# Optimization experiments

Measured on AMD Instinct MI355X. Metric: run time of the kernel, lower is better.

Reference implementation:

```python
import jax, jax.numpy as jnp
import numpy as np

K_TOP = 4          # self.k
NUM_EXPERTS = 16   # self.num_experts
LOSS_COEF = 0.01


def setup_inputs() -> dict:
    key = jax.random.key(0)
    k0, k1, k2, k3, k4 = jax.random.split(key, 5)
    B, Cin, Cout, H, Wd, E = 16, 64, 64, 64, 64, NUM_EXPERTS
    x = jax.random.normal(k0, (B, Cin, H, Wd), dtype=jnp.float32)
    w_gate = jax.random.normal(k1, (Cin, E), dtype=jnp.float32) * 0.1
    w_noise = jax.random.normal(k2, (Cin, E), dtype=jnp.float32) * 0.1
    W = jax.random.normal(k3, (E, Cout, Cin, 3, 3), dtype=jnp.float32) * (1.0 / np.sqrt(Cin * 9).astype(np.float32))
    b = jax.random.normal(k4, (E, Cout), dtype=jnp.float32) * 0.01
    return {"x": x, "w_gate": w_gate, "w_noise": w_noise, "W": W, "b": b, "train": 0}


def _cv_squared(v):
    # torch .var() is unbiased (ddof=1)
    v = v.astype(jnp.float32)
    return jnp.var(v, ddof=1) / (jnp.mean(v) ** 2 + 1e-10)


def reference(x, w_gate, w_noise, W, b, train):
    B = x.shape[0]
    E = NUM_EXPERTS
    # gate_x = flatten(avgpool(x)) -> [B, Cin]
    gate_x = jnp.mean(x, axis=(2, 3))
    clean_logits = gate_x @ w_gate                      # [B, E]
    # train == 0 (eval): no noise branch; logits = softmax(clean_logits)
    logits = jax.nn.softmax(clean_logits, axis=1)
    top_vals, top_idx = jax.lax.top_k(logits, min(K_TOP + 1, E))
    tk_vals = top_vals[:, :K_TOP]                       # [B, k]
    tk_idx = top_idx[:, :K_TOP]                         # [B, k]
    tk_gates = tk_vals / (jnp.sum(tk_vals, axis=1, keepdims=True) + 1e-6)
    gates = jnp.zeros_like(logits).at[jnp.arange(B)[:, None], tk_idx].set(tk_gates)  # [B, E]
    # load (eval path): count of nonzero gates per expert
    load = jax.lax.stop_gradient(jnp.sum(gates > 0, axis=0)).astype(jnp.float32)     # [E]
    importance = jnp.sum(gates, axis=0)                 # [E]
    loss = (_cv_squared(importance) + _cv_squared(load)) * LOSS_COEF
    # dispatch/combine == dense gated mixture: zero-gate experts contribute 0.
    def conv_one(w):
        return jax.lax.conv_general_dilated(
            x, w, window_strides=(1, 1), padding=[(1, 1), (1, 1)],
            dimension_numbers=("NCHW", "OIHW", "NCHW"))
    expert_outs = jax.vmap(conv_one)(W) + b[:, None, :, None, None]  # [E, B, Cout, H, W]
    y = jnp.einsum("ebchw,be->bchw", expert_outs, gates)
    return (y, loss)
```

## Files before the change

kernel.cpp:

```cpp
#include <hip/hip_runtime.h>
#include <hip/hip_bf16.h>


typedef __attribute__((ext_vector_type(8))) short bf16x8;
typedef __attribute__((ext_vector_type(4))) float f32x4;

__device__ inline unsigned short f2bf(float f) {
  unsigned u = __builtin_bit_cast(unsigned, f);
  unsigned r = u + 0x7FFFu + ((u >> 16) & 1u);
  return (unsigned short)(r >> 16);
}

__global__ __launch_bounds__(256) void transpose_kernel(const float* __restrict__ x,
                                                        unsigned short* __restrict__ xt,
                                                        float* __restrict__ gpart) {
  int bh = blockIdx.x;
  int b = bh >> 6, h = bh & 63;
  __shared__ float tile[64][65];
  int t = threadIdx.x;
  const float4* xrow = (const float4*)(x + ((size_t)b * 64 * 64 + h) * 64) ;
#pragma unroll
  for (int k = 0; k < 4; ++k) {
    int idx = t + k * 256;
    int ci = idx >> 4;
    int w4 = idx & 15;
    float4 v = *(const float4*)(x + ((((size_t)b * 64 + ci) * 64 + h) * 64 + w4 * 4));
    tile[ci][w4 * 4 + 0] = v.x;
    tile[ci][w4 * 4 + 1] = v.y;
    tile[ci][w4 * 4 + 2] = v.z;
    tile[ci][w4 * 4 + 3] = v.w;
  }
  (void)xrow;
  __syncthreads();
  if (t < 64) {
    float s = 0.f;
#pragma unroll
    for (int w2 = 0; w2 < 64; ++w2) s += tile[t][w2];
    gpart[(size_t)bh * 64 + t] = s;
  }
#pragma unroll
  for (int it = 0; it < 2; ++it) {
    int idx = t + it * 256;
    int g = idx >> 6;
    int wo = idx & 63;
    bf16x8 v;
#pragma unroll
    for (int j = 0; j < 8; ++j) v[j] = (short)f2bf(tile[g * 8 + j][wo]);
    *(bf16x8*)(xt + (((size_t)bh * 8 + g) * 64 + wo) * 8) = v;
  }
}

__device__ inline void softmax_top4(const float* sl, float* gv, int* ge) {
  float m = sl[0];
#pragma unroll
  for (int i = 1; i < 16; ++i) m = fmaxf(m, sl[i]);
  float p[16];
  float z = 0.f;
#pragma unroll
  for (int i = 0; i < 16; ++i) { p[i] = expf(sl[i] - m); z += p[i]; }
#pragma unroll
  for (int i = 0; i < 16; ++i) p[i] /= z;
  bool used[16];
#pragma unroll
  for (int i = 0; i < 16; ++i) used[i] = false;
  float val[4];
  for (int j = 0; j < 4; ++j) {
    int bi = 0; float bv = -1.f;
    for (int i = 0; i < 16; ++i)
      if (!used[i] && p[i] > bv) { bv = p[i]; bi = i; }
    used[bi] = true; ge[j] = bi; val[j] = bv;
  }
  float ssum = val[0] + val[1] + val[2] + val[3] + 1e-6f;
  for (int j = 0; j < 4; ++j) gv[j] = val[j] / ssum;
}

__global__ __launch_bounds__(256) void combine_gate_kernel(const float* __restrict__ gpart,
                                                           const float* __restrict__ w_gate,
                                                           const float* __restrict__ W,
                                                           const float* __restrict__ bias,
                                                           unsigned short* __restrict__ wc,
                                                           float* __restrict__ bc,
                                                           float* __restrict__ loss_out) {
  int cog = blockIdx.x;
  int b = blockIdx.y;
  int t = threadIdx.x;

  if (cog == 16) {
    if (b != 0) return;
    __shared__ float red[4][64];
    __shared__ float sgx[16][64];
    __shared__ float sl[16][16];
    __shared__ float sg[16][16];
    __shared__ float simp[16], sld[16];
    int hg = t >> 6, ci = t & 63;
    for (int bb = 0; bb < 16; ++bb) {
      float s = 0.f;
#pragma unroll
      for (int hh = 0; hh < 16; ++hh)
        s += gpart[((size_t)(bb * 64 + hg * 16 + hh)) * 64 + ci];
      red[hg][ci] = s;
      __syncthreads();
      if (t < 64) sgx[bb][t] = (red[0][t] + red[1][t] + red[2][t] + red[3][t]) * (1.0f / 4096.0f);
      __syncthreads();
    }
    {
      int bb = t >> 4, e = t & 15;
      float acc = 0.f;
      for (int c = 0; c < 64; ++c) acc += sgx[bb][c] * w_gate[c * 16 + e];
      sl[bb][e] = acc;
    }
    __syncthreads();
    if (t < 16) {
      float gv[4]; int ge[4];
      softmax_top4(sl[t], gv, ge);
#pragma unroll
      for (int i = 0; i < 16; ++i) sg[t][i] = 0.f;
      for (int j = 0; j < 4; ++j) sg[t][ge[j]] = gv[j];
    }
    __syncthreads();
    if (t < 16) {
      int ee = t; float imp = 0.f, ld = 0.f;
      for (int bb = 0; bb < 16; ++bb) {
        float g = sg[bb][ee];
        imp += g;
        if (g > 0.f) ld += 1.f;
      }
      simp[ee] = imp; sld[ee] = ld;
    }
    __syncthreads();
    if (t == 0) {
      float mi = 0.f, ml = 0.f;
      for (int i = 0; i < 16; ++i) { mi += simp[i]; ml += sld[i]; }
      mi *= (1.f / 16.f); ml *= (1.f / 16.f);
      float vi = 0.f, vl = 0.f;
      for (int i = 0; i < 16; ++i) {
        float d = simp[i] - mi; vi += d * d;
        float dl = sld[i] - ml; vl += dl * dl;
      }
      vi *= (1.f / 15.f); vl *= (1.f / 15.f);
      loss_out[0] = (vi / (mi * mi + 1e-10f) + vl / (ml * ml + 1e-10f)) * 0.01f;
    }
    return;
  }

  __shared__ float red[4][64];
  __shared__ float sgx[64];
  __shared__ float sl[16];
  __shared__ float g[4];
  __shared__ int e[4];
  __shared__ float was[2304];
  {
    int hg = t >> 6, ci = t & 63;
    float s = 0.f;
#pragma unroll
    for (int hh = 0; hh < 16; ++hh)
      s += gpart[((size_t)(b * 64 + hg * 16 + hh)) * 64 + ci];
    red[hg][ci] = s;
  }
  __syncthreads();
  if (t < 64) sgx[t] = (red[0][t] + red[1][t] + red[2][t] + red[3][t]) * (1.0f / 4096.0f);
  __syncthreads();
  if (t < 16) {
    float acc = 0.f;
    for (int c = 0; c < 64; ++c) acc += sgx[c] * w_gate[c * 16 + t];
    sl[t] = acc;
  }
  __syncthreads();
  if (t == 0) {
    float gv[4]; int ge[4];
    softmax_top4(sl, gv, ge);
#pragma unroll
    for (int j = 0; j < 4; ++j) { g[j] = gv[j]; e[j] = ge[j]; }
  }
  __syncthreads();
  float g0 = g[0], g1 = g[1], g2 = g[2], g3 = g[3];
  int e0 = e[0], e1 = e[1], e2 = e[2], e3 = e[3];
  if (cog == 0 && t < 64)
    bc[b * 64 + t] = g0 * bias[e0 * 64 + t] + g1 * bias[e1 * 64 + t] +
                     g2 * bias[e2 * 64 + t] + g3 * bias[e3 * 64 + t];
  const float* b0 = W + e0 * 36864 + cog * 2304;
  const float* b1 = W + e1 * 36864 + cog * 2304;
  const float* b2 = W + e2 * 36864 + cog * 2304;
  const float* b3 = W + e3 * 36864 + cog * 2304;
  float acc[9];
#pragma unroll
  for (int j = 0; j < 9; ++j) {
    int o = t + j * 256;
    acc[j] = g0 * b0[o] + g1 * b1[o] + g2 * b2[o] + g3 * b3[o];
  }
#pragma unroll
  for (int j = 0; j < 9; ++j) was[t + j * 256] = acc[j];
  __syncthreads();
  for (int v = t; v < 288; v += 256) {
    int co_l = v & 3, gg = (v >> 2) & 7, p = v >> 5;
    bf16x8 ov;
#pragma unroll
    for (int j = 0; j < 8; ++j)
      ov[j] = (short)f2bf(was[co_l * 576 + (gg * 8 + j) * 9 + p]);
    *(bf16x8*)(wc + (size_t)b * 36864 + ((p * 8 + gg) * 64 + cog * 4 + co_l) * 8) = ov;
  }
}

__global__ __launch_bounds__(512) void conv_mfma(const unsigned short* __restrict__ xt,
                                                 const unsigned short* __restrict__ wc,
                                                 const float* __restrict__ bc,
                                                 float* __restrict__ y) {
  int rt = blockIdx.x;
  int b = blockIdx.y;
  int tid = threadIdx.x;
  int wv = tid >> 6, L = tid & 63;
  int lane15 = L & 15, quad = L >> 4;
  int row = rt * 4 + (wv >> 1);
  int colbase = (wv & 1) * 32;
  const unsigned short* xtb = xt + ((size_t)b << 18);
  const unsigned short* wcb = wc + (size_t)b * 36864;
  f32x4 acc[4][2];
#pragma unroll
  for (int mt = 0; mt < 4; ++mt)
#pragma unroll
    for (int nt = 0; nt < 2; ++nt) acc[mt][nt] = (f32x4){0.f, 0.f, 0.f, 0.f};
  const bf16x8 zero = {0, 0, 0, 0, 0, 0, 0, 0};
#pragma unroll
  for (int p = 0; p < 9; ++p) {
    int dr = p / 3, dc = p % 3;
    int h = row + dr - 1;
    bool hok = (unsigned)h < 64u;
#pragma unroll
    for (int ck = 0; ck < 2; ++ck) {
      int g = ck * 4 + quad;
      bf16x8 bfr[2];
#pragma unroll
      for (int nt = 0; nt < 2; ++nt) {
        int w = colbase + nt * 16 + lane15 + dc - 1;
        bf16x8 v = zero;
        if (hok && (unsigned)w < 64u)
          v = *(const bf16x8*)(xtb + (((h << 3) + g) << 9) + (w << 3));
        bfr[nt] = v;
      }
      bf16x8 afr[4];
#pragma unroll
      for (int mt = 0; mt < 4; ++mt)
        afr[mt] = *(const bf16x8*)(wcb + ((((p << 3) + g) << 6) + mt * 16 + lane15) * 8);
#pragma unroll
      for (int mt = 0; mt < 4; ++mt)
#pragma unroll
        for (int nt = 0; nt < 2; ++nt)
          acc[mt][nt] = __builtin_amdgcn_mfma_f32_16x16x32_bf16(afr[mt], bfr[nt], acc[mt][nt], 0, 0, 0);
    }
  }
#pragma unroll
  for (int mt = 0; mt < 4; ++mt) {
#pragma unroll
    for (int r = 0; r < 4; ++r) {
      int co = mt * 16 + quad * 4 + r;
      float bias = bc[(b << 6) + co];
#pragma unroll
      for (int nt = 0; nt < 2; ++nt) {
        int w = colbase + nt * 16 + lane15;
        y[(((size_t)(b << 6) + co) << 12) + (row << 6) + w] = acc[mt][nt][r] + bias;
      }
    }
  }
}

extern "C" void kernel_launch(void* const* d_in, const int* in_sizes, int n_in,
                              void* d_out, int out_size, void* d_ws, size_t ws_size,
                              hipStream_t stream) {
  const float* x = (const float*)d_in[0];
  const float* w_gate = (const float*)d_in[1];
  const float* W = (const float*)d_in[3];
  const float* bias = (const float*)d_in[4];
  float* out = (float*)d_out;
  float* ws = (float*)d_ws;

  float* gpart = ws;
  float* bc = ws + 65536;
  unsigned short* wc = (unsigned short*)(ws + 66560);
  unsigned short* xt = (unsigned short*)(ws + 361472);

  transpose_kernel<<<1024, 256, 0, stream>>>(x, xt, gpart);
  {
    dim3 grid(17, 16);
    combine_gate_kernel<<<grid, 256, 0, stream>>>(gpart, w_gate, W, bias, wc, bc,
                                                  out + 4194304);
  }
  {
    dim3 grid(16, 16);
    conv_mfma<<<grid, 512, 0, stream>>>(xt, wc, bc, out);
  }
}
```

Baseline: 106.8 us.

## Fuse transpose, gating, and conv into one cooperative kernel with grid syncs

Replaces the three separate kernel launches (transpose+pool, gate/weight combine, MFMA conv) with a single cooperative kernel of 256 blocks that separates the phases with grid.sync(). Each block now transposes four rows instead of one, and one block also computes the loss after the combine phase. This removes the launch gaps between kernels. In exchange it adds two grid-wide barriers, cuts parallelism in the transpose phase to 256 blocks, and puts the serial loss computation on the critical path before the second sync.

```diff
diff --git a/kernel.cpp b/kernel.cpp
--- a/kernel.cpp
+++ b/kernel.cpp
@@ -1,5 +1,8 @@
 #include <hip/hip_runtime.h>
 #include <hip/hip_bf16.h>
+#include <hip/hip_cooperative_groups.h>
+
+namespace cg = cooperative_groups;
 
 
 typedef __attribute__((ext_vector_type(8))) short bf16x8;
@@ -9,45 +12,6 @@
   unsigned u = __builtin_bit_cast(unsigned, f);
   unsigned r = u + 0x7FFFu + ((u >> 16) & 1u);
   return (unsigned short)(r >> 16);
-}
-
-__global__ __launch_bounds__(256) void transpose_kernel(const float* __restrict__ x,
-                                                        unsigned short* __restrict__ xt,
-                                                        float* __restrict__ gpart) {
-  int bh = blockIdx.x;
-  int b = bh >> 6, h = bh & 63;
-  __shared__ float tile[64][65];
-  int t = threadIdx.x;
-  const float4* xrow = (const float4*)(x + ((size_t)b * 64 * 64 + h) * 64) ;
-#pragma unroll
-  for (int k = 0; k < 4; ++k) {
-    int idx = t + k * 256;
-    int ci = idx >> 4;
-    int w4 = idx & 15;
-    float4 v = *(const float4*)(x + ((((size_t)b * 64 + ci) * 64 + h) * 64 + w4 * 4));
-    tile[ci][w4 * 4 + 0] = v.x;
-    tile[ci][w4 * 4 + 1] = v.y;
-    tile[ci][w4 * 4 + 2] = v.z;
-    tile[ci][w4 * 4 + 3] = v.w;
-  }
-  (void)xrow;
-  __syncthreads();
-  if (t < 64) {
-    float s = 0.f;
-#pragma unroll
-    for (int w2 = 0; w2 < 64; ++w2) s += tile[t][w2];
-    gpart[(size_t)bh * 64 + t] = s;
-  }
-#pragma unroll
-  for (int it = 0; it < 2; ++it) {
-    int idx = t + it * 256;
-    int g = idx >> 6;
-    int wo = idx & 63;
-    bf16x8 v;
-#pragma unroll
-    for (int j = 0; j < 8; ++j) v[j] = (short)f2bf(tile[g * 8 + j][wo]);
-    *(bf16x8*)(xt + (((size_t)bh * 8 + g) * 64 + wo) * 8) = v;
-  }
 }
 
 __device__ inline void softmax_top4(const float* sl, float* gv, int* ge) {
@@ -74,36 +38,137 @@
   for (int j = 0; j < 4; ++j) gv[j] = val[j] / ssum;
 }
 
-__global__ __launch_bounds__(256) void combine_gate_kernel(const float* __restrict__ gpart,
-                                                           const float* __restrict__ w_gate,
-                                                           const float* __restrict__ W,
-                                                           const float* __restrict__ bias,
-                                                           unsigned short* __restrict__ wc,
-                                                           float* __restrict__ bc,
-                                                           float* __restrict__ loss_out) {
-  int cog = blockIdx.x;
-  int b = blockIdx.y;
+__global__ __launch_bounds__(512) void fused_kernel(
+    const float* __restrict__ x, const float* __restrict__ w_gate,
+    const float* __restrict__ W, const float* __restrict__ bias,
+    unsigned short* __restrict__ xt, unsigned short* __restrict__ wc,
+    float* __restrict__ gpart, float* __restrict__ bc,
+    float* __restrict__ y, float* __restrict__ loss_out) {
+  cg::grid_group grid = cg::this_grid();
+  int blk = blockIdx.x;
   int t = threadIdx.x;
 
-  if (cog == 16) {
-    if (b != 0) return;
-    __shared__ float red[4][64];
-    __shared__ float sgx[16][64];
-    __shared__ float sl[16][16];
-    __shared__ float sg[16][16];
-    __shared__ float simp[16], sld[16];
-    int hg = t >> 6, ci = t & 63;
+  __shared__ float tile[64][65];
+  __shared__ float red[8][64];
+  __shared__ float sgx[16][64];
+  __shared__ float sl[16][16];
+  __shared__ float sg[16][16];
+  __shared__ float simp[16], sld[16];
+  __shared__ float gsh[4];
+  __shared__ int esh[4];
+  __shared__ float was[2304];
+
+#pragma unroll
+  for (int u = 0; u < 4; ++u) {
+    int bh = blk * 4 + u;
+    int b = bh >> 6, h = bh & 63;
+    __syncthreads();
+#pragma unroll
+    for (int k = 0; k < 2; ++k) {
+      int idx = t + k * 512;
+      int ci = idx >> 4;
+      int w4 = idx & 15;
+      float4 v = *(const float4*)(x + ((((size_t)b * 64 + ci) * 64 + h) * 64 + w4 * 4));
+      tile[ci][w4 * 4 + 0] = v.x;
+      tile[ci][w4 * 4 + 1] = v.y;
+      tile[ci][w4 * 4 + 2] = v.z;
+      tile[ci][w4 * 4 + 3] = v.w;
+    }
+    __syncthreads();
+    if (t < 64) {
+      float s = 0.f;
+#pragma unroll
+      for (int w2 = 0; w2 < 64; ++w2) s += tile[t][w2];
+      gpart[(size_t)bh * 64 + t] = s;
+    }
+    {
+      int g = t >> 6, wo = t & 63;
+      bf16x8 v;
+#pragma unroll
+      for (int j = 0; j < 8; ++j) v[j] = (short)f2bf(tile[g * 8 + j][wo]);
+      *(bf16x8*)(xt + (((size_t)bh * 8 + g) * 64 + wo) * 8) = v;
+    }
+  }
+
+  grid.sync();
+
+  {
+    int cog = blk & 15, b = blk >> 4;
+    {
+      int hg = t >> 6, ci = t & 63;
+      float s = 0.f;
+#pragma unroll
+      for (int hh = 0; hh < 8; ++hh)
+        s += gpart[((size_t)(b * 64 + hg * 8 + hh)) * 64 + ci];
+      red[hg][ci] = s;
+    }
+    __syncthreads();
+    if (t < 64) {
+      float s = 0.f;
+#pragma unroll
+      for (int i = 0; i < 8; ++i) s += red[i][t];
+      sgx[0][t] = s * (1.0f / 4096.0f);
+    }
+    __syncthreads();
+    if (t < 16) {
+      float acc = 0.f;
+      for (int c = 0; c < 64; ++c) acc += sgx[0][c] * w_gate[c * 16 + t];
+      sl[0][t] = acc;
+    }
+    __syncthreads();
+    if (t == 0) {
+      float gv[4]; int ge[4];
+      softmax_top4(sl[0], gv, ge);
+#pragma unroll
+      for (int j = 0; j < 4; ++j) { gsh[j] = gv[j]; esh[j] = ge[j]; }
+    }
+    __syncthreads();
+    float g0 = gsh[0], g1 = gsh[1], g2 = gsh[2], g3 = gsh[3];
+    int e0 = esh[0], e1 = esh[1], e2 = esh[2], e3 = esh[3];
+    if (cog == 0 && t < 64)
+      bc[b * 64 + t] = g0 * bias[e0 * 64 + t] + g1 * bias[e1 * 64 + t] +
+                       g2 * bias[e2 * 64 + t] + g3 * bias[e3 * 64 + t];
+    const float* b0 = W + e0 * 36864 + cog * 2304;
+    const float* b1 = W + e1 * 36864 + cog * 2304;
+    const float* b2 = W + e2 * 36864 + cog * 2304;
+    const float* b3 = W + e3 * 36864 + cog * 2304;
+#pragma unroll
+    for (int j = 0; j < 5; ++j) {
+      int o = t + j * 512;
+      if (o < 2304) was[o] = g0 * b0[o] + g1 * b1[o] + g2 * b2[o] + g3 * b3[o];
+    }
+    __syncthreads();
+    if (t < 288) {
+      int co_l = t & 3, gg = (t >> 2) & 7, p = t >> 5;
+      bf16x8 ov;
+#pragma unroll
+      for (int j = 0; j < 8; ++j)
+        ov[j] = (short)f2bf(was[co_l * 576 + (gg * 8 + j) * 9 + p]);
+      *(bf16x8*)(wc + (size_t)b * 36864 + ((p * 8 + gg) * 64 + cog * 4 + co_l) * 8) = ov;
+    }
+  }
+
+  if (blk == 255) {
+    __syncthreads();
     for (int bb = 0; bb < 16; ++bb) {
-      float s = 0.f;
-#pragma unroll
-      for (int hh = 0; hh < 16; ++hh)
-        s += gpart[((size_t)(bb * 64 + hg * 16 + hh)) * 64 + ci];
-      red[hg][ci] = s;
+      {
+        int hg = t >> 6, ci = t & 63;
+        float s = 0.f;
+#pragma unroll
+        for (int hh = 0; hh < 8; ++hh)
+          s += gpart[((size_t)(bb * 64 + hg * 8 + hh)) * 64 + ci];
+        red[hg][ci] = s;
+      }
       __syncthreads();
-      if (t < 64) sgx[bb][t] = (red[0][t] + red[1][t] + red[2][t] + red[3][t]) * (1.0f / 4096.0f);
+      if (t < 64) {
+        float s = 0.f;
+#pragma unroll
+        for (int i = 0; i < 8; ++i) s += red[i][t];
+        sgx[bb][t] = s * (1.0f / 4096.0f);
+      }
       __syncthreads();
     }
-    {
+    if (t < 256) {
       int bb = t >> 4, e = t & 15;
       float acc = 0.f;
       for (int c = 0; c < 64; ++c) acc += sgx[bb][c] * w_gate[c * 16 + e];
@@ -140,124 +205,64 @@
       vi *= (1.f / 15.f); vl *= (1.f / 15.f);
       loss_out[0] = (vi / (mi * mi + 1e-10f) + vl / (ml * ml + 1e-10f)) * 0.01f;
     }
-    return;
-  }
-
-  __shared__ float red[4][64];
-  __shared__ float sgx[64];
-  __shared__ float sl[16];
-  __shared__ float g[4];
-  __shared__ int e[4];
-  __shared__ float was[2304];
+  }
+
+  grid.sync();
+
   {
-    int hg = t >> 6, ci = t & 63;
-    float s = 0.f;
-#pragma unroll
-    for (int hh = 0; hh < 16; ++hh)
-      s += gpart[((size_t)(b * 64 + hg * 16 + hh)) * 64 + ci];
-    red[hg][ci] = s;
-  }
-  __syncthreads();
-  if (t < 64) sgx[t] = (red[0][t] + red[1][t] + red[2][t] + red[3][t]) * (1.0f / 4096.0f);
-  __syncthreads();
-  if (t < 16) {
-    float acc = 0.f;
-    for (int c = 0; c < 64; ++c) acc += sgx[c] * w_gate[c * 16 + t];
-    sl[t] = acc;
-  }
-  __syncthreads();
-  if (t == 0) {
-    float gv[4]; int ge[4];
-    softmax_top4(sl, gv, ge);
-#pragma unroll
-    for (int j = 0; j < 4; ++j) { g[j] = gv[j]; e[j] = ge[j]; }
-  }
-  __syncthreads();
-  float g0 = g[0], g1 = g[1], g2 = g[2], g3 = g[3];
-  int e0 = e[0], e1 = e[1], e2 = e[2], e3 = e[3];
-  if (cog == 0 && t < 64)
-    bc[b * 64 + t] = g0 * bias[e0 * 64 + t] + g1 * bias[e1 * 64 + t] +
-                     g2 * bias[e2 * 64 + t] + g3 * bias[e3 * 64 + t];
-  const float* b0 = W + e0 * 36864 + cog * 2304;
-  const float* b1 = W + e1 * 36864 + cog * 2304;
-  const float* b2 = W + e2 * 36864 + cog * 2304;
-  const float* b3 = W + e3 * 36864 + cog * 2304;
-  float acc[9];
-#pragma unroll
-  for (int j = 0; j < 9; ++j) {
-    int o = t + j * 256;
-    acc[j] = g0 * b0[o] + g1 * b1[o] + g2 * b2[o] + g3 * b3[o];
-  }
-#pragma unroll
-  for (int j = 0; j < 9; ++j) was[t + j * 256] = acc[j];
-  __syncthreads();
-  for (int v = t; v < 288; v += 256) {
-    int co_l = v & 3, gg = (v >> 2) & 7, p = v >> 5;
-    bf16x8 ov;
-#pragma unroll
-    for (int j = 0; j < 8; ++j)
-      ov[j] = (short)f2bf(was[co_l * 576 + (gg * 8 + j) * 9 + p]);
-    *(bf16x8*)(wc + (size_t)b * 36864 + ((p * 8 + gg) * 64 + cog * 4 + co_l) * 8) = ov;
-  }
-}
-
-__global__ __launch_bounds__(512) void conv_mfma(const unsigned short* __restrict__ xt,
-                                                 const unsigned short* __restrict__ wc,
-                                                 const float* __restrict__ bc,
-                                                 float* __restrict__ y) {
-  int rt = blockIdx.x;
-  int b = blockIdx.y;
-  int tid = threadIdx.x;
-  int wv = tid >> 6, L = tid & 63;
-  int lane15 = L & 15, quad = L >> 4;
-  int row = rt * 4 + (wv >> 1);
-  int colbase = (wv & 1) * 32;
-  const unsigned short* xtb = xt + ((size_t)b << 18);
-  const unsigned short* wcb = wc + (size_t)b * 36864;
-  f32x4 acc[4][2];
-#pragma unroll
-  for (int mt = 0; mt < 4; ++mt)
-#pragma unroll
-    for (int nt = 0; nt < 2; ++nt) acc[mt][nt] = (f32x4){0.f, 0.f, 0.f, 0.f};
-  const bf16x8 zero = {0, 0, 0, 0, 0, 0, 0, 0};
-#pragma unroll
-  for (int p = 0; p < 9; ++p) {
-    int dr = p / 3, dc = p % 3;
-    int h = row + dr - 1;
-    bool hok = (unsigned)h < 64u;
-#pragma unroll
-    for (int ck = 0; ck < 2; ++ck) {
-      int g = ck * 4 + quad;
-      bf16x8 bfr[2];
-#pragma unroll
-      for (int nt = 0; nt < 2; ++nt) {
-        int w = colbase + nt * 16 + lane15 + dc - 1;
-        bf16x8 v = zero;
-        if (hok && (unsigned)w < 64u)
-          v = *(const bf16x8*)(xtb + (((h << 3) + g) << 9) + (w << 3));
-        bfr[nt] = v;
-      }
-      bf16x8 afr[4];
-#pragma unroll
-      for (int mt = 0; mt < 4; ++mt)
-        afr[mt] = *(const bf16x8*)(wcb + ((((p << 3) + g) << 6) + mt * 16 + lane15) * 8);
-#pragma unroll
-      for (int mt = 0; mt < 4; ++mt)
-#pragma unroll
-        for (int nt = 0; nt < 2; ++nt)
-          acc[mt][nt] = __builtin_amdgcn_mfma_f32_16x16x32_bf16(afr[mt], bfr[nt], acc[mt][nt], 0, 0, 0);
-    }
-  }
-#pragma unroll
-  for (int mt = 0; mt < 4; ++mt) {
-#pragma unroll
-    for (int r = 0; r < 4; ++r) {
-      int co = mt * 16 + quad * 4 + r;
-      float bias = bc[(b << 6) + co];
-#pragma unroll
-      for (int nt = 0; nt < 2; ++nt) {
-        int w = colbase + nt * 16 + lane15;
-        y[(((size_t)(b << 6) + co) << 12) + (row << 6) + w] = acc[mt][nt][r] + bias;
+    int rt = blk & 15;
+    int b = blk >> 4;
+    int wv = t >> 6, L = t & 63;
+    int lane15 = L & 15, quad = L >> 4;
+    int row = rt * 4 + (wv >> 1);
+    int colbase = (wv & 1) * 32;
+    const unsigned short* xtb = xt + ((size_t)b << 18);
+    const unsigned short* wcb = wc + (size_t)b * 36864;
+    f32x4 acc[4][2];
+#pragma unroll
+    for (int mt = 0; mt < 4; ++mt)
+#pragma unroll
+      for (int nt = 0; nt < 2; ++nt) acc[mt][nt] = (f32x4){0.f, 0.f, 0.f, 0.f};
+    const bf16x8 zero = {0, 0, 0, 0, 0, 0, 0, 0};
+#pragma unroll
+    for (int p = 0; p < 9; ++p) {
+      int dr = p / 3, dc = p % 3;
+      int h = row + dr - 1;
+      bool hok = (unsigned)h < 64u;
+#pragma unroll
+      for (int ck = 0; ck < 2; ++ck) {
+        int g = ck * 4 + quad;
+        bf16x8 bfr[2];
+#pragma unroll
+        for (int nt = 0; nt < 2; ++nt) {
+          int w = colbase + nt * 16 + lane15 + dc - 1;
+          bf16x8 v = zero;
+          if (hok && (unsigned)w < 64u)
+            v = *(const bf16x8*)(xtb + (((h << 3) + g) << 9) + (w << 3));
+          bfr[nt] = v;
+        }
+        bf16x8 afr[4];
+#pragma unroll
+        for (int mt = 0; mt < 4; ++mt)
+          afr[mt] = *(const bf16x8*)(wcb + ((((p << 3) + g) << 6) + mt * 16 + lane15) * 8);
+#pragma unroll
+        for (int mt = 0; mt < 4; ++mt)
+#pragma unroll
+          for (int nt = 0; nt < 2; ++nt)
+            acc[mt][nt] = __builtin_amdgcn_mfma_f32_16x16x32_bf16(afr[mt], bfr[nt], acc[mt][nt], 0, 0, 0);
+      }
+    }
+#pragma unroll
+    for (int mt = 0; mt < 4; ++mt) {
+#pragma unroll
+      for (int r = 0; r < 4; ++r) {
+        int co = mt * 16 + quad * 4 + r;
+        float bv = bc[(b << 6) + co];
+#pragma unroll
+        for (int nt = 0; nt < 2; ++nt) {
+          int w = colbase + nt * 16 + lane15;
+          y[(((size_t)(b << 6) + co) << 12) + (row << 6) + w] = acc[mt][nt][r] + bv;
+        }
       }
     }
   }
@@ -277,15 +282,11 @@
   float* bc = ws + 65536;
   unsigned short* wc = (unsigned short*)(ws + 66560);
   unsigned short* xt = (unsigned short*)(ws + 361472);
-
-  transpose_kernel<<<1024, 256, 0, stream>>>(x, xt, gpart);
-  {
-    dim3 grid(17, 16);
-    combine_gate_kernel<<<grid, 256, 0, stream>>>(gpart, w_gate, W, bias, wc, bc,
-                                                  out + 4194304);
-  }
-  {
-    dim3 grid(16, 16);
-    conv_mfma<<<grid, 512, 0, stream>>>(xt, wc, bc, out);
-  }
-}
+  float* loss_out = out + 4194304;
+
+  void* args[] = {(void*)&x, (void*)&w_gate, (void*)&W, (void*)&bias,
+                  (void*)&xt, (void*)&wc, (void*)&gpart, (void*)&bc,
+                  (void*)&out, (void*)&loss_out};
+  hipLaunchCooperativeKernel((void*)fused_kernel, dim3(256), dim3(512), args, 0,
+                             stream);
+}
```

New measurement: 185.0 us. +73.3%, slower.
